# Kernel tuning notes

Hardware: AMD Instinct MI355X
Metric: run time of the kernel (lower is better)

## Reference

```python
import jax, jax.numpy as jnp
import numpy as np

B, I, H1, H2, E, T = 16384, 512, 256, 128, 8, 2


def setup_inputs() -> dict:
    key = jax.random.key(0)
    ks = jax.random.split(key, 4)
    # Xavier-ish scaling for stability
    x = jax.random.normal(ks[0], (B, I), dtype=jnp.float32)
    W1 = jax.random.normal(ks[1], (E, I, H1), dtype=jnp.float32) / np.sqrt(I)
    b1 = jnp.zeros((E, H1), dtype=jnp.float32)
    W2 = jax.random.normal(ks[2], (E, H1, H2), dtype=jnp.float32) / np.sqrt(H1)
    b2 = jnp.zeros((E, H2), dtype=jnp.float32)
    Wg = jax.random.normal(ks[3], (T, I, E), dtype=jnp.float32) / np.sqrt(I)
    bg = jnp.zeros((T, E), dtype=jnp.float32)
    return {"x": x, "W1": W1, "b1": b1, "W2": W2, "b2": b2, "Wg": Wg, "bg": bg}


def reference(x, W1, b1, W2, b2, Wg, bg):
    # All experts as one grouped GEMM: [E, B, H1]
    h = jax.nn.relu(jnp.einsum('bi,eih->ebh', x, W1) + b1[:, None, :])
    # Last expert layer (lastlayer_reg=True -> act applied): [E, B, H2]
    e_out = jax.nn.relu(jnp.einsum('ebh,eho->ebo', h, W2) + b2[:, None, :])
    # Per-task gates with softmax over experts: [T, B, E]
    gates = jax.nn.softmax(jnp.einsum('bi,tie->tbe', x, Wg) + bg[:, None, :], axis=-1)
    # Gate-weighted combine of expert outputs: [T, B, H2]
    towers = jnp.einsum('tbe,ebo->tbo', gates, e_out)
    return towers
```

## Files before the change

### kernel.cpp

```cpp
#include <hip/hip_runtime.h>
#include <hip/hip_bf16.h>

#define B_  16384
#define I_  512
#define H1_ 256
#define H2_ 128
#define E_  8
#define T_  2

typedef __attribute__((ext_vector_type(8))) short short8;
typedef __attribute__((ext_vector_type(4))) float float4_t;

__device__ inline unsigned short f2bf(float f) {
    union { float f; unsigned u; } v; v.f = f;
    unsigned r = v.u + 0x7FFFu + ((v.u >> 16) & 1u);
    return (unsigned short)(r >> 16);
}

__device__ inline void async_copy16(const unsigned short* g, unsigned short* l) {
    __builtin_amdgcn_global_load_lds(
        (const __attribute__((address_space(1))) void*)g,
        (__attribute__((address_space(3))) void*)l,
        16, 0, 0);
}

__global__ void prep_gates_kernel(const float* __restrict__ x,
                                  unsigned short* __restrict__ xb,
                                  const float* __restrict__ W1,
                                  unsigned short* __restrict__ w1t,
                                  const float* __restrict__ W2,
                                  unsigned short* __restrict__ w2t,
                                  const float* __restrict__ Wg,
                                  const float* __restrict__ bg,
                                  float* __restrict__ gates) {
    __shared__ __align__(16) char smem[16 * 520 * 2 + 4 * 16 * 16 * 4];
    int bid = blockIdx.x;
    int t = threadIdx.x;

    if (bid < 1024) {
        unsigned short* wgtL = (unsigned short*)smem;
        float (*red)[16][16] = (float (*)[16][16])(smem + 16 * 520 * 2);
#pragma unroll
        for (int j = 0; j < 32; ++j) {
            int idx = j * 256 + t;
            int e = idx & 7, i = (idx >> 3) & 511, task = idx >> 12;
            wgtL[(task * 8 + e) * 520 + i] = f2bf(Wg[idx]);
        }
        __syncthreads();

        int w = t >> 6, lane = t & 63;
        int col = lane & 15, quad = lane >> 4;
        int b0 = bid * 16;
        int k0 = w * 128;
        const float* xr = x + (size_t)(b0 + col) * I_ + k0 + quad * 8;
        unsigned short* xw = xb + (size_t)(b0 + col) * I_ + k0 + quad * 8;
        const unsigned short* bL = &wgtL[col * 520 + k0 + quad * 8];
        float4_t acc = {0.f, 0.f, 0.f, 0.f};
#pragma unroll
        for (int ks = 0; ks < 128; ks += 32) {
            float4_t xa = *(const float4_t*)(xr + ks);
            float4_t xc = *(const float4_t*)(xr + ks + 4);
            short8 a;
            a[0] = (short)f2bf(xa[0]); a[1] = (short)f2bf(xa[1]);
            a[2] = (short)f2bf(xa[2]); a[3] = (short)f2bf(xa[3]);
            a[4] = (short)f2bf(xc[0]); a[5] = (short)f2bf(xc[1]);
            a[6] = (short)f2bf(xc[2]); a[7] = (short)f2bf(xc[3]);
            *(short8*)(xw + ks) = a;
            short8 b = *(const short8*)(bL + ks);
            acc = __builtin_amdgcn_mfma_f32_16x16x32_bf16(a, b, acc, 0, 0, 0);
        }
#pragma unroll
        for (int p = 0; p < 4; ++p)
            red[w][quad * 4 + p][col] = acc[p];
        __syncthreads();
        int r = t >> 4, te = t & 15;
        float v = red[0][r][te] + red[1][r][te] + red[2][r][te] + red[3][r][te] + bg[te];
        float m = v;
        m = fmaxf(m, __shfl_xor(m, 1));
        m = fmaxf(m, __shfl_xor(m, 2));
        m = fmaxf(m, __shfl_xor(m, 4));
        float ev = __expf(v - m);
        float s = ev;
        s += __shfl_xor(s, 1);
        s += __shfl_xor(s, 2);
        s += __shfl_xor(s, 4);
        gates[(size_t)te * B_ + b0 + r] = ev / s;
    } else {
        float (*tile)[33] = (float (*)[33])smem;
        const float* in; unsigned short* outp; int R, C, e, r0, c0;
        if (bid < 2048) {
            int tl = bid - 1024;
            e = tl >> 7; int rem = tl & 127;
            R = I_; C = H1_;
            r0 = (rem >> 3) * 32; c0 = (rem & 7) * 32;
            in = W1; outp = w1t;
        } else {
            int tl = bid - 2048;
            e = tl >> 5; int rem = tl & 31;
            R = H1_; C = H2_;
            r0 = (rem >> 2) * 32; c0 = (rem & 3) * 32;
            in = W2; outp = w2t;
        }
        const float* inp = in + (size_t)e * R * C;
        unsigned short* op = outp + (size_t)e * R * C;
        int tx = t & 31, ty = t >> 5;
#pragma unroll
        for (int j = 0; j < 32; j += 8)
            tile[ty + j][tx] = inp[(size_t)(r0 + ty + j) * C + c0 + tx];
        __syncthreads();
#pragma unroll
        for (int j = 0; j < 32; j += 8)
            op[(size_t)(c0 + ty + j) * R + r0 + tx] = f2bf(tile[tx][ty + j]);
    }
}

__global__ void gemm_relu_kernel(const unsigned short* __restrict__ A, size_t aSE,
                                 const unsigned short* __restrict__ Bt, size_t bSE,
                                 const float* __restrict__ bias, int biasSE,
                                 unsigned short* __restrict__ C, size_t cSE,
                                 int K, int lda, int ldb, int ldc) {
    __shared__ unsigned short smem[128 * 136];
    unsigned short* As = smem;
    unsigned short* Bs = smem + 128 * 64;
    int e = blockIdx.z;
    const unsigned short* Ae = A + (size_t)e * aSE;
    const unsigned short* Be = Bt + (size_t)e * bSE;
    const float* biasE = bias + (size_t)e * biasSE;
    unsigned short* Ce = C + (size_t)e * cSE;
    int m0 = blockIdx.x * 128, n0 = blockIdx.y * 128;
    int t = threadIdx.x, w = t >> 6, lane = t & 63;
    int col = lane & 15, quad = lane >> 4;
    int wm = (w & 1) * 64, wn = (w >> 1) * 64;

    float4_t acc[4][4];
#pragma unroll
    for (int mi = 0; mi < 4; ++mi)
#pragma unroll
        for (int ni = 0; ni < 4; ++ni)
            acc[mi][ni] = (float4_t){0.f, 0.f, 0.f, 0.f};

    int rT = t >> 3;
    int gk = (((t & 7) ^ (rT & 7))) * 8;
    const unsigned short* aG = Ae + (size_t)(m0 + rT) * lda + gk;
    const unsigned short* bG = Be + (size_t)(n0 + rT) * ldb + gk;
    unsigned short* aL = As + (size_t)w * 64 * 8;
    unsigned short* bL = Bs + (size_t)w * 64 * 8;

    for (int k0 = 0; k0 < K; k0 += 64) {
#pragma unroll
        for (int j = 0; j < 4; ++j) {
            async_copy16(aG + (size_t)j * 32 * lda + k0, aL + j * 2048);
            async_copy16(bG + (size_t)j * 32 * ldb + k0, bL + j * 2048);
        }
        __syncthreads();
#pragma unroll
        for (int kk = 0; kk < 64; kk += 32) {
            int q = (kk >> 3) + quad;
            short8 af[4], bf[4];
#pragma unroll
            for (int mi = 0; mi < 4; ++mi) {
                int r = wm + mi * 16 + col;
                af[mi] = *(const short8*)&As[r * 64 + ((q ^ (r & 7)) * 8)];
            }
#pragma unroll
            for (int ni = 0; ni < 4; ++ni) {
                int r = wn + ni * 16 + col;
                bf[ni] = *(const short8*)&Bs[r * 64 + ((q ^ (r & 7)) * 8)];
            }
#pragma unroll
            for (int mi = 0; mi < 4; ++mi)
#pragma unroll
                for (int ni = 0; ni < 4; ++ni)
                    acc[mi][ni] = __builtin_amdgcn_mfma_f32_16x16x32_bf16(af[mi], bf[ni], acc[mi][ni], 0, 0, 0);
        }
        __syncthreads();
    }
    unsigned short* Ct = smem;
#pragma unroll
    for (int ni = 0; ni < 4; ++ni) {
        int c = wn + ni * 16 + col;
        float bv = biasE[n0 + c];
#pragma unroll
        for (int mi = 0; mi < 4; ++mi) {
            int rbase = wm + mi * 16 + quad * 4;
#pragma unroll
            for (int p = 0; p < 4; ++p) {
                float v = acc[mi][ni][p] + bv;
                v = v > 0.f ? v : 0.f;
                Ct[(rbase + p) * 136 + c] = f2bf(v);
            }
        }
    }
    __syncthreads();
    int rr = t >> 4, sl = t & 15;
#pragma unroll
    for (int pass = 0; pass < 8; ++pass) {
        int row = pass * 16 + rr;
        short8 vv = *(const short8*)&Ct[row * 136 + sl * 8];
        *(short8*)&Ce[(size_t)(m0 + row) * ldc + n0 + sl * 8] = vv;
    }
}

__global__ void fused_l2_combine_kernel(const unsigned short* __restrict__ h,
                                        const unsigned short* __restrict__ w2t,
                                        const float* __restrict__ b2,
                                        const float* __restrict__ gates,
                                        float* __restrict__ out) {
    __shared__ unsigned short As[64 * 256];
    __shared__ unsigned short Bs[64 * 256];
    __shared__ float gL[16][64];

    int b0 = blockIdx.x * 64;
    int nh = blockIdx.y * 64;
    int t = threadIdx.x, w = t >> 6, lane = t & 63;
    int col = lane & 15, quad = lane >> 4;
    int wm = (w & 1) * 32, wn = (w >> 1) * 32;

    {
        int te = t >> 4, r4 = (t & 15) * 4;
        *(float4_t*)&gL[te][r4] = *(const float4_t*)&gates[(size_t)te * B_ + b0 + r4];
    }

    float4_t tw0[2][2], tw1[2][2];
#pragma unroll
    for (int mi = 0; mi < 2; ++mi)
#pragma unroll
        for (int ni = 0; ni < 2; ++ni) {
            tw0[mi][ni] = (float4_t){0.f, 0.f, 0.f, 0.f};
            tw1[mi][ni] = (float4_t){0.f, 0.f, 0.f, 0.f};
        }

    int rL = w * 2 + (lane >> 5);
    int cL = lane & 31;

    for (int e = 0; e < E_; ++e) {
        const unsigned short* hE = h + ((size_t)e * B_ + b0) * H1_;
        const unsigned short* w2E = w2t + ((size_t)e * H2_ + nh) * H1_;

#pragma unroll
        for (int j = 0; j < 8; ++j) {
            int r = j * 8 + rL;
            int cg = (cL & 24) | ((cL ^ r) & 7);
            async_copy16(hE + (size_t)r * H1_ + cg * 8, As + j * 2048 + w * 512);
            async_copy16(w2E + (size_t)r * H1_ + cg * 8, Bs + j * 2048 + w * 512);
        }
        __syncthreads();

        float4_t acc[2][2];
#pragma unroll
        for (int mi = 0; mi < 2; ++mi)
#pragma unroll
            for (int ni = 0; ni < 2; ++ni)
                acc[mi][ni] = (float4_t){0.f, 0.f, 0.f, 0.f};

#pragma unroll
        for (int kk = 0; kk < 8; ++kk) {
            int c = kk * 4 + quad;
            short8 af[2], bf[2];
#pragma unroll
            for (int mi = 0; mi < 2; ++mi) {
                int r = wm + mi * 16 + col;
                int l = (c & 24) | ((c ^ r) & 7);
                af[mi] = *(const short8*)&As[r * 256 + l * 8];
            }
#pragma unroll
            for (int ni = 0; ni < 2; ++ni) {
                int r = wn + ni * 16 + col;
                int l = (c & 24) | ((c ^ r) & 7);
                bf[ni] = *(const short8*)&Bs[r * 256 + l * 8];
            }
#pragma unroll
            for (int mi = 0; mi < 2; ++mi)
#pragma unroll
                for (int ni = 0; ni < 2; ++ni)
                    acc[mi][ni] = __builtin_amdgcn_mfma_f32_16x16x32_bf16(af[mi], bf[ni], acc[mi][ni], 0, 0, 0);
        }
        __syncthreads();

#pragma unroll
        for (int ni = 0; ni < 2; ++ni) {
            float bv = b2[e * H2_ + nh + wn + ni * 16 + col];
#pragma unroll
            for (int mi = 0; mi < 2; ++mi) {
#pragma unroll
                for (int p = 0; p < 4; ++p) {
                    int rloc = wm + mi * 16 + quad * 4 + p;
                    float v = acc[mi][ni][p] + bv;
                    v = v > 0.f ? v : 0.f;
                    tw0[mi][ni][p] += gL[e][rloc] * v;
                    tw1[mi][ni][p] += gL[8 + e][rloc] * v;
                }
            }
        }
    }

#pragma unroll
    for (int mi = 0; mi < 2; ++mi) {
#pragma unroll
        for (int ni = 0; ni < 2; ++ni) {
            int n = nh + wn + ni * 16 + col;
#pragma unroll
            for (int p = 0; p < 4; ++p) {
                int r = b0 + wm + mi * 16 + quad * 4 + p;
                out[(size_t)r * H2_ + n] = tw0[mi][ni][p];
                out[(size_t)B_ * H2_ + (size_t)r * H2_ + n] = tw1[mi][ni][p];
            }
        }
    }
}

extern "C" void kernel_launch(void* const* d_in, const int* in_sizes, int n_in,
                              void* d_out, int out_size, void* d_ws, size_t ws_size,
                              hipStream_t stream) {
    const float* x  = (const float*)d_in[0];
    const float* W1 = (const float*)d_in[1];
    const float* b1 = (const float*)d_in[2];
    const float* W2 = (const float*)d_in[3];
    const float* b2 = (const float*)d_in[4];
    const float* Wg = (const float*)d_in[5];
    const float* bg = (const float*)d_in[6];
    float* out = (float*)d_out;

    char* ws = (char*)d_ws;
    unsigned short* xb    = (unsigned short*)(ws);
    unsigned short* w1t   = (unsigned short*)(ws + 16777216);
    unsigned short* w2t   = (unsigned short*)(ws + 18874368);
    float*          gates = (float*)(ws + 19398656);
    unsigned short* h     = (unsigned short*)(ws + 20447232);

    prep_gates_kernel<<<dim3(2304), 256, 0, stream>>>(x, xb, W1, w1t, W2, w2t, Wg, bg, gates);

    gemm_relu_kernel<<<dim3(B_ / 128, H1_ / 128, E_), 256, 0, stream>>>(
        xb, 0, w1t, (size_t)H1_ * I_, b1, H1_, h, (size_t)B_ * H1_, I_, I_, I_, H1_);

    fused_l2_combine_kernel<<<dim3(B_ / 64, 2), 256, 0, stream>>>(h, w2t, b2, gates, out);
}
```

Before: 160.6 us.

## Pipeline layer-2 combine with 3-slot async ring, shrink GEMM LDS, vectorize Wg load

The fused layer-2/combine kernel now covers all 128 output columns per block with 512 threads, so h is read once instead of twice. It streams K-chunks through a three-slot LDS ring with async global-to-LDS copies and explicit vmcnt waits, raising MFMA priority during compute. The layer-1 GEMM epilogue is split into two halves so its LDS drops to 32KB, and it gets launch bounds for higher occupancy. The gate-weight transpose uses float4 loads. The cost is more barriers in the GEMM epilogue and a hand-managed wait-count pipeline that is easy to get wrong.

```diff
diff --git a/kernel.cpp b/kernel.cpp
--- a/kernel.cpp
+++ b/kernel.cpp
@@ -41,10 +41,15 @@
         unsigned short* wgtL = (unsigned short*)smem;
         float (*red)[16][16] = (float (*)[16][16])(smem + 16 * 520 * 2);
 #pragma unroll
-        for (int j = 0; j < 32; ++j) {
-            int idx = j * 256 + t;
-            int e = idx & 7, i = (idx >> 3) & 511, task = idx >> 12;
-            wgtL[(task * 8 + e) * 520 + i] = f2bf(Wg[idx]);
+        for (int j = 0; j < 8; ++j) {
+            int idx4 = j * 256 + t;
+            float4_t wv = ((const float4_t*)Wg)[idx4];
+            int e0   = (idx4 & 1) * 4;
+            int i    = (idx4 >> 1) & 511;
+            int task = idx4 >> 10;
+#pragma unroll
+            for (int c = 0; c < 4; ++c)
+                wgtL[(task * 8 + e0 + c) * 520 + i] = f2bf(wv[c]);
         }
         __syncthreads();
 
@@ -114,14 +119,15 @@
     }
 }
 
-__global__ void gemm_relu_kernel(const unsigned short* __restrict__ A, size_t aSE,
-                                 const unsigned short* __restrict__ Bt, size_t bSE,
-                                 const float* __restrict__ bias, int biasSE,
-                                 unsigned short* __restrict__ C, size_t cSE,
-                                 int K, int lda, int ldb, int ldc) {
-    __shared__ unsigned short smem[128 * 136];
+__global__ __launch_bounds__(256, 5)
+void gemm_relu_kernel(const unsigned short* __restrict__ A, size_t aSE,
+                      const unsigned short* __restrict__ Bt, size_t bSE,
+                      const float* __restrict__ bias, int biasSE,
+                      unsigned short* __restrict__ C, size_t cSE,
+                      int K, int lda, int ldb, int ldc) {
+    __shared__ __align__(16) unsigned short smem[16384];
     unsigned short* As = smem;
-    unsigned short* Bs = smem + 128 * 64;
+    unsigned short* Bs = smem + 8192;
     int e = blockIdx.z;
     const unsigned short* Ae = A + (size_t)e * aSE;
     const unsigned short* Be = Bt + (size_t)e * bSE;
@@ -177,49 +183,61 @@
     }
     unsigned short* Ct = smem;
 #pragma unroll
-    for (int ni = 0; ni < 4; ++ni) {
-        int c = wn + ni * 16 + col;
-        float bv = biasE[n0 + c];
-#pragma unroll
-        for (int mi = 0; mi < 4; ++mi) {
-            int rbase = wm + mi * 16 + quad * 4;
-#pragma unroll
-            for (int p = 0; p < 4; ++p) {
-                float v = acc[mi][ni][p] + bv;
-                v = v > 0.f ? v : 0.f;
-                Ct[(rbase + p) * 136 + c] = f2bf(v);
-            }
-        }
-    }
-    __syncthreads();
-    int rr = t >> 4, sl = t & 15;
-#pragma unroll
-    for (int pass = 0; pass < 8; ++pass) {
-        int row = pass * 16 + rr;
-        short8 vv = *(const short8*)&Ct[row * 136 + sl * 8];
-        *(short8*)&Ce[(size_t)(m0 + row) * ldc + n0 + sl * 8] = vv;
-    }
-}
-
-__global__ void fused_l2_combine_kernel(const unsigned short* __restrict__ h,
-                                        const unsigned short* __restrict__ w2t,
-                                        const float* __restrict__ b2,
-                                        const float* __restrict__ gates,
-                                        float* __restrict__ out) {
-    __shared__ unsigned short As[64 * 256];
-    __shared__ unsigned short Bs[64 * 256];
+    for (int half = 0; half < 2; ++half) {
+        if ((w & 1) == half) {
+#pragma unroll
+            for (int ni = 0; ni < 4; ++ni) {
+                int c = wn + ni * 16 + col;
+                float bv = biasE[n0 + c];
+#pragma unroll
+                for (int mi = 0; mi < 4; ++mi) {
+                    int rl = mi * 16 + quad * 4;
+#pragma unroll
+                    for (int p = 0; p < 4; ++p) {
+                        float v = acc[mi][ni][p] + bv;
+                        v = v > 0.f ? v : 0.f;
+                        Ct[(rl + p) * 136 + c] = f2bf(v);
+                    }
+                }
+            }
+        }
+        __syncthreads();
+        int rr = t >> 4, sl = t & 15;
+#pragma unroll
+        for (int pass = 0; pass < 4; ++pass) {
+            int row = pass * 16 + rr;
+            short8 vv = *(const short8*)&Ct[row * 136 + sl * 8];
+            *(short8*)&Ce[(size_t)(m0 + half * 64 + row) * ldc + n0 + sl * 8] = vv;
+        }
+        __syncthreads();
+    }
+}
+
+__global__ __launch_bounds__(512, 4)
+void fused_l2_combine_kernel(const unsigned short* __restrict__ h,
+                             const unsigned short* __restrict__ w2t,
+                             const float* __restrict__ b2,
+                             const float* __restrict__ gates,
+                             float* __restrict__ out) {
+    __shared__ __align__(16) unsigned short ring[36864];
     __shared__ float gL[16][64];
 
+    unsigned short* Aslot = ring;
+    unsigned short* Bslot = ring + 12288;
+
     int b0 = blockIdx.x * 64;
-    int nh = blockIdx.y * 64;
     int t = threadIdx.x, w = t >> 6, lane = t & 63;
     int col = lane & 15, quad = lane >> 4;
     int wm = (w & 1) * 32, wn = (w >> 1) * 32;
 
-    {
+    if (t < 256) {
         int te = t >> 4, r4 = (t & 15) * 4;
         *(float4_t*)&gL[te][r4] = *(const float4_t*)&gates[(size_t)te * B_ + b0 + r4];
     }
+
+    int rowA = t >> 3;
+    int csw  = ((t & 7) ^ (rowA & 7)) * 8;
+    int ldsw = w * 512;
 
     float4_t tw0[2][2], tw1[2][2];
 #pragma unroll
@@ -230,75 +248,89 @@
             tw1[mi][ni] = (float4_t){0.f, 0.f, 0.f, 0.f};
         }
 
-    int rL = w * 2 + (lane >> 5);
-    int cL = lane & 31;
-
-    for (int e = 0; e < E_; ++e) {
-        const unsigned short* hE = h + ((size_t)e * B_ + b0) * H1_;
-        const unsigned short* w2E = w2t + ((size_t)e * H2_ + nh) * H1_;
-
-#pragma unroll
-        for (int j = 0; j < 8; ++j) {
-            int r = j * 8 + rL;
-            int cg = (cL & 24) | ((cL ^ r) & 7);
-            async_copy16(hE + (size_t)r * H1_ + cg * 8, As + j * 2048 + w * 512);
-            async_copy16(w2E + (size_t)r * H1_ + cg * 8, Bs + j * 2048 + w * 512);
-        }
-        __syncthreads();
-
-        float4_t acc[2][2];
-#pragma unroll
-        for (int mi = 0; mi < 2; ++mi)
-#pragma unroll
-            for (int ni = 0; ni < 2; ++ni)
-                acc[mi][ni] = (float4_t){0.f, 0.f, 0.f, 0.f};
-
-#pragma unroll
-        for (int kk = 0; kk < 8; ++kk) {
-            int c = kk * 4 + quad;
-            short8 af[2], bf[2];
+    auto stage = [&](int cid, int slot) {
+        int ee = cid >> 2, kc = cid & 3;
+        const unsigned short* hE = h + ((size_t)ee * B_ + b0 + rowA) * H1_ + kc * 64 + csw;
+        async_copy16(hE, Aslot + slot * 4096 + ldsw);
+        const unsigned short* wE = w2t + ((size_t)ee * H2_ + rowA) * H1_ + kc * 64 + csw;
+        async_copy16(wE, Bslot + slot * 8192 + ldsw);
+        async_copy16(wE + (size_t)64 * H1_, Bslot + slot * 8192 + 4096 + ldsw);
+    };
+
+    stage(0, 0);
+
+    float4_t acc[2][2];
+    int rd = 0, wr = 1;
+#pragma unroll 1
+    for (int cid = 0; cid < 32; ++cid) {
+        if (cid < 31) {
+            stage(cid + 1, wr);
+            asm volatile("s_waitcnt vmcnt(3)" ::: "memory");
+        } else {
+            asm volatile("s_waitcnt vmcnt(0)" ::: "memory");
+        }
+        asm volatile("s_barrier" ::: "memory");
+
+        if ((cid & 3) == 0) {
+#pragma unroll
+            for (int mi = 0; mi < 2; ++mi)
+#pragma unroll
+                for (int ni = 0; ni < 2; ++ni)
+                    acc[mi][ni] = (float4_t){0.f, 0.f, 0.f, 0.f};
+        }
+        const unsigned short* Ac = Aslot + rd * 4096;
+        const unsigned short* Bc = Bslot + rd * 8192;
+#pragma unroll
+        for (int kq = 0; kq < 2; ++kq) {
+            int q = kq * 4 + quad;
+            short8 af[2], bfv[2];
 #pragma unroll
             for (int mi = 0; mi < 2; ++mi) {
                 int r = wm + mi * 16 + col;
-                int l = (c & 24) | ((c ^ r) & 7);
-                af[mi] = *(const short8*)&As[r * 256 + l * 8];
+                af[mi] = *(const short8*)&Ac[r * 64 + ((q ^ (r & 7)) << 3)];
             }
 #pragma unroll
             for (int ni = 0; ni < 2; ++ni) {
-                int r = wn + ni * 16 + col;
-                int l = (c & 24) | ((c ^ r) & 7);
-                bf[ni] = *(const short8*)&Bs[r * 256 + l * 8];
-            }
+                int n = wn + ni * 16 + col;
+                bfv[ni] = *(const short8*)&Bc[n * 64 + ((q ^ (n & 7)) << 3)];
+            }
+            __builtin_amdgcn_s_setprio(1);
 #pragma unroll
             for (int mi = 0; mi < 2; ++mi)
 #pragma unroll
                 for (int ni = 0; ni < 2; ++ni)
-                    acc[mi][ni] = __builtin_amdgcn_mfma_f32_16x16x32_bf16(af[mi], bf[ni], acc[mi][ni], 0, 0, 0);
-        }
-        __syncthreads();
-
+                    acc[mi][ni] = __builtin_amdgcn_mfma_f32_16x16x32_bf16(
+                        af[mi], bfv[ni], acc[mi][ni], 0, 0, 0);
+            __builtin_amdgcn_s_setprio(0);
+        }
+
+        if ((cid & 3) == 3) {
+            int ee = cid >> 2;
+#pragma unroll
+            for (int ni = 0; ni < 2; ++ni) {
+                float bv = b2[ee * H2_ + wn + ni * 16 + col];
+#pragma unroll
+                for (int mi = 0; mi < 2; ++mi) {
+#pragma unroll
+                    for (int p = 0; p < 4; ++p) {
+                        int rloc = wm + mi * 16 + quad * 4 + p;
+                        float v = acc[mi][ni][p] + bv;
+                        v = v > 0.f ? v : 0.f;
+                        tw0[mi][ni][p] += gL[ee][rloc] * v;
+                        tw1[mi][ni][p] += gL[8 + ee][rloc] * v;
+                    }
+                }
+            }
+        }
+        rd = (rd == 2) ? 0 : rd + 1;
+        wr = (wr == 2) ? 0 : wr + 1;
+    }
+
+#pragma unroll
+    for (int mi = 0; mi < 2; ++mi) {
 #pragma unroll
         for (int ni = 0; ni < 2; ++ni) {
-            float bv = b2[e * H2_ + nh + wn + ni * 16 + col];
-#pragma unroll
-            for (int mi = 0; mi < 2; ++mi) {
-#pragma unroll
-                for (int p = 0; p < 4; ++p) {
-                    int rloc = wm + mi * 16 + quad * 4 + p;
-                    float v = acc[mi][ni][p] + bv;
-                    v = v > 0.f ? v : 0.f;
-                    tw0[mi][ni][p] += gL[e][rloc] * v;
-                    tw1[mi][ni][p] += gL[8 + e][rloc] * v;
-                }
-            }
-        }
-    }
-
-#pragma unroll
-    for (int mi = 0; mi < 2; ++mi) {
-#pragma unroll
-        for (int ni = 0; ni < 2; ++ni) {
-            int n = nh + wn + ni * 16 + col;
+            int n = wn + ni * 16 + col;
 #pragma unroll
             for (int p = 0; p < 4; ++p) {
                 int r = b0 + wm + mi * 16 + quad * 4 + p;
@@ -333,5 +365,5 @@
     gemm_relu_kernel<<<dim3(B_ / 128, H1_ / 128, E_), 256, 0, stream>>>(
         xb, 0, w1t, (size_t)H1_ * I_, b1, H1_, h, (size_t)B_ * H1_, I_, I_, I_, H1_);
 
-    fused_l2_combine_kernel<<<dim3(B_ / 64, 2), 256, 0, stream>>>(h, w2t, b2, gates, out);
-}
+    fused_l2_combine_kernel<<<dim3(B_ / 64), 512, 0, stream>>>(h, w2t, b2, gates, out);
+}
```

Measured after the change: 250.8 us. +56.1%, slower.
